# Kernel tuning notes

Measured on AMD Instinct MI355X. Metric: run time of the kernel, lower is better.

## Reference

```python
import jax, jax.numpy as jnp
import numpy as np

N_VIDEOS = 256
EMBED_DIM = 1024
MARGIN = 0.0

def _segment_sizes():
    i = np.arange(N_VIDEOS)
    num_clips = 8 + (i % 17)            # sum = 4088
    num_caps = 8 + ((5 * i + 3) % 17)   # sum = 4091
    return num_clips, num_caps

def setup_inputs() -> dict:
    key = jax.random.key(0)
    num_clips, num_caps = _segment_sizes()
    total_clips = int(num_clips.sum())
    total_caps = int(num_caps.sum())
    k1, k2 = jax.random.split(key)
    im = jax.random.normal(k1, (total_clips, EMBED_DIM), dtype=jnp.float32)
    s = jax.random.normal(k2, (total_caps, EMBED_DIM), dtype=jnp.float32)
    return {
        "im": im,
        "s": s,
        "num_clips": jnp.asarray(num_clips, jnp.int32),
        "num_caps": jnp.asarray(num_caps, jnp.int32),
    }

def reference(im, s, num_clips, num_caps):
    N = num_clips.shape[0]
    # full similarity matrix [total_clips, total_caps]
    scores = im @ s.T
    # segment ids mapping each clip/caption row to its video group
    clip_seg = jnp.repeat(jnp.arange(N), num_clips, total_repeat_length=im.shape[0])
    cap_seg = jnp.repeat(jnp.arange(N), num_caps, total_repeat_length=s.shape[0])
    # two-stage segmented sum -> block sums [N, N], then divide for block means
    row_red = jax.ops.segment_sum(scores, clip_seg, num_segments=N)       # [N, total_caps]
    blk_sum = jax.ops.segment_sum(row_red.T, cap_seg, num_segments=N).T   # [N, N]
    counts = num_clips.astype(jnp.float32)[:, None] * num_caps.astype(jnp.float32)[None, :]
    S = blk_sum / counts
    diag = jnp.diag(S)
    cost_s = jnp.maximum(MARGIN + S - diag[:, None], 0.0)   # caption retrieval
    cost_im = jnp.maximum(MARGIN + S - diag[None, :], 0.0)  # image retrieval
    eye = jnp.eye(N, dtype=bool)
    cost_s = jnp.where(eye, 0.0, cost_s)
    cost_im = jnp.where(eye, 0.0, cost_im)
    return cost_s.sum() + cost_im.sum()
```

## Files before the change

kernel.cpp:

```cpp
#include <hip/hip_runtime.h>

#define NVID 256
#define DIM 1024

__device__ inline void acc4(float4& a, const float4& v) {
    a.x += v.x; a.y += v.y; a.z += v.z; a.w += v.w;
}

__global__ __launch_bounds__(256) void seg_mean_kernel(
    const float* __restrict__ im, const float* __restrict__ s,
    const int* __restrict__ num_clips, const int* __restrict__ num_caps,
    float* __restrict__ A, float* __restrict__ B, float* __restrict__ out)
{
    const int b = blockIdx.x;
    const int t = threadIdx.x;
    if (b == 0 && t == 0) out[0] = 0.0f;

    const bool isClip = (b < NVID);
    const int vid = isClip ? b : b - NVID;
    const int* cnt = isClip ? num_clips : num_caps;
    const float* src = isClip ? im : s;
    float* dst = isClip ? A : B;

    __shared__ int scnt[NVID];
    scnt[t] = cnt[t];
    __syncthreads();

    int off = 0;
    for (int k = 0; k < vid; ++k) off += scnt[k];
    const int n = scnt[vid];

    const float4* srcv = (const float4*)src + (size_t)off * (DIM / 4) + t;
    float4 a0 = {0,0,0,0}, a1 = {0,0,0,0}, a2 = {0,0,0,0}, a3 = {0,0,0,0};
    int r = 0;
    for (; r + 4 <= n; r += 4) {
        float4 v0 = srcv[(size_t)(r + 0) * (DIM / 4)];
        float4 v1 = srcv[(size_t)(r + 1) * (DIM / 4)];
        float4 v2 = srcv[(size_t)(r + 2) * (DIM / 4)];
        float4 v3 = srcv[(size_t)(r + 3) * (DIM / 4)];
        acc4(a0, v0); acc4(a1, v1); acc4(a2, v2); acc4(a3, v3);
    }
    for (; r < n; ++r) {
        float4 v = srcv[(size_t)r * (DIM / 4)];
        acc4(a0, v);
    }
    acc4(a0, a1); acc4(a2, a3); acc4(a0, a2);
    const float inv = 1.0f / (float)n;
    a0.x *= inv; a0.y *= inv; a0.z *= inv; a0.w *= inv;
    ((float4*)(dst + (size_t)vid * DIM))[t] = a0;
}

__global__ __launch_bounds__(256) void diag_kernel(
    const float* __restrict__ A, const float* __restrict__ B,
    float* __restrict__ diag)
{
    const int i = blockIdx.x;
    const int t = threadIdx.x;
    float4 a = ((const float4*)(A + (size_t)i * DIM))[t];
    float4 b = ((const float4*)(B + (size_t)i * DIM))[t];
    float p = a.x * b.x + a.y * b.y + a.z * b.z + a.w * b.w;

    for (int o = 32; o > 0; o >>= 1) p += __shfl_down(p, o, 64);

    __shared__ float wsum[4];
    const int wave = t >> 6, lane = t & 63;
    if (lane == 0) wsum[wave] = p;
    __syncthreads();
    if (t == 0) diag[i] = wsum[0] + wsum[1] + wsum[2] + wsum[3];
}

__global__ __launch_bounds__(256) void loss_kernel(
    const float* __restrict__ A, const float* __restrict__ B,
    const float* __restrict__ diag, float* __restrict__ out)
{
    constexpr int KC = 64;
    constexpr int LDW = KC + 4;
    __shared__ float As[2][16][LDW];
    __shared__ float Bs[2][16][LDW];

    const int t = threadIdx.x;
    const int tx = t & 15, ty = t >> 4;
    const int i0 = blockIdx.y * 16, j0 = blockIdx.x * 16;

    const int lrow = t >> 4;
    const int lcol = (t & 15) * 4;

    const float* Arow = A + (size_t)(i0 + lrow) * DIM + lcol;
    const float* Brow = B + (size_t)(j0 + lrow) * DIM + lcol;

    float4 va = *(const float4*)(Arow + 0);
    float4 vb = *(const float4*)(Brow + 0);
    *(float4*)&As[0][lrow][lcol] = va;
    *(float4*)&Bs[0][lrow][lcol] = vb;
    __syncthreads();

    float acc = 0.f;
    constexpr int NCHUNK = DIM / KC;
    for (int c = 0; c < NCHUNK; ++c) {
        const int cur = c & 1;
        if (c + 1 < NCHUNK) {
            va = *(const float4*)(Arow + (c + 1) * KC);
            vb = *(const float4*)(Brow + (c + 1) * KC);
        }
#pragma unroll
        for (int k = 0; k < KC; k += 4) {
            float4 fa = *(const float4*)&As[cur][ty][k];
            float4 fb = *(const float4*)&Bs[cur][tx][k];
            acc += fa.x * fb.x + fa.y * fb.y + fa.z * fb.z + fa.w * fb.w;
        }
        if (c + 1 < NCHUNK) {
            *(float4*)&As[cur ^ 1][lrow][lcol] = va;
            *(float4*)&Bs[cur ^ 1][lrow][lcol] = vb;
        }
        __syncthreads();
    }

    const int i = i0 + ty, j = j0 + tx;
    float v = 0.f;
    if (i != j) {
        const float dI = diag[i];
        const float dJ = diag[j];
        v = fmaxf(acc - dI, 0.f) + fmaxf(acc - dJ, 0.f);
    }

    for (int o = 32; o > 0; o >>= 1) v += __shfl_down(v, o, 64);
    __shared__ float wsum[4];
    const int wave = t >> 6, lane = t & 63;
    if (lane == 0) wsum[wave] = v;
    __syncthreads();
    if (t == 0) atomicAdd(out, wsum[0] + wsum[1] + wsum[2] + wsum[3]);
}

extern "C" void kernel_launch(void* const* d_in, const int* in_sizes, int n_in,
                              void* d_out, int out_size, void* d_ws, size_t ws_size,
                              hipStream_t stream) {
    const float* im    = (const float*)d_in[0];
    const float* s     = (const float*)d_in[1];
    const int*   nclip = (const int*)d_in[2];
    const int*   ncap  = (const int*)d_in[3];
    float* out = (float*)d_out;

    float* A    = (float*)d_ws;
    float* B    = A + NVID * DIM;
    float* diag = B + NVID * DIM;

    seg_mean_kernel<<<2 * NVID, 256, 0, stream>>>(im, s, nclip, ncap, A, B, out);
    diag_kernel<<<NVID, 256, 0, stream>>>(A, B, diag);
    loss_kernel<<<dim3(16, 16), 256, 0, stream>>>(A, B, diag, out);
}
```

Measured before the change: 95.53 us.

## Store segment means as bf16 and compute block scores with MFMA

Segment-mean rows are now stored in bf16, and the 256x256 score GEMM is done by one wave per 16x16 tile using the 16x16x32 bf16 MFMA instruction instead of an LDS-tiled FP32 dot-product loop. The diag kernel reads the same bf16 values, so diagonal and off-diagonal scores stay consistent. The segment-mean loop is also unrolled to eight rows per iteration. The aim is less workspace traffic and faster matrix-core math in the loss kernel. The cost is bf16 rounding of the means, which may perturb the hinge sum since the margin is zero.

```diff
diff --git a/kernel.cpp b/kernel.cpp
--- a/kernel.cpp
+++ b/kernel.cpp
@@ -1,16 +1,32 @@
 #include <hip/hip_runtime.h>
+#include <hip/hip_bf16.h>
 
 #define NVID 256
 #define DIM 1024
+
+typedef short bf16x8 __attribute__((ext_vector_type(8)));
+typedef float f32x4 __attribute__((ext_vector_type(4)));
 
 __device__ inline void acc4(float4& a, const float4& v) {
     a.x += v.x; a.y += v.y; a.z += v.z; a.w += v.w;
 }
 
+__device__ inline unsigned short f2bf(float f) {
+    __hip_bfloat16 h = __float2bfloat16(f);
+    unsigned short u;
+    __builtin_memcpy(&u, &h, 2);
+    return u;
+}
+
+__device__ inline float bf2f(unsigned short u) {
+    return __uint_as_float(((unsigned)u) << 16);
+}
+
 __global__ __launch_bounds__(256) void seg_mean_kernel(
     const float* __restrict__ im, const float* __restrict__ s,
     const int* __restrict__ num_clips, const int* __restrict__ num_caps,
-    float* __restrict__ A, float* __restrict__ B, float* __restrict__ out)
+    unsigned short* __restrict__ Ab, unsigned short* __restrict__ Bb,
+    float* __restrict__ out)
 {
     const int b = blockIdx.x;
     const int t = threadIdx.x;
@@ -20,7 +36,7 @@
     const int vid = isClip ? b : b - NVID;
     const int* cnt = isClip ? num_clips : num_caps;
     const float* src = isClip ? im : s;
-    float* dst = isClip ? A : B;
+    unsigned short* dst = isClip ? Ab : Bb;
 
     __shared__ int scnt[NVID];
     scnt[t] = cnt[t];
@@ -33,12 +49,17 @@
     const float4* srcv = (const float4*)src + (size_t)off * (DIM / 4) + t;
     float4 a0 = {0,0,0,0}, a1 = {0,0,0,0}, a2 = {0,0,0,0}, a3 = {0,0,0,0};
     int r = 0;
-    for (; r + 4 <= n; r += 4) {
+    for (; r + 8 <= n; r += 8) {
         float4 v0 = srcv[(size_t)(r + 0) * (DIM / 4)];
         float4 v1 = srcv[(size_t)(r + 1) * (DIM / 4)];
         float4 v2 = srcv[(size_t)(r + 2) * (DIM / 4)];
         float4 v3 = srcv[(size_t)(r + 3) * (DIM / 4)];
+        float4 v4 = srcv[(size_t)(r + 4) * (DIM / 4)];
+        float4 v5 = srcv[(size_t)(r + 5) * (DIM / 4)];
+        float4 v6 = srcv[(size_t)(r + 6) * (DIM / 4)];
+        float4 v7 = srcv[(size_t)(r + 7) * (DIM / 4)];
         acc4(a0, v0); acc4(a1, v1); acc4(a2, v2); acc4(a3, v3);
+        acc4(a0, v4); acc4(a1, v5); acc4(a2, v6); acc4(a3, v7);
     }
     for (; r < n; ++r) {
         float4 v = srcv[(size_t)r * (DIM / 4)];
@@ -47,18 +68,22 @@
     acc4(a0, a1); acc4(a2, a3); acc4(a0, a2);
     const float inv = 1.0f / (float)n;
     a0.x *= inv; a0.y *= inv; a0.z *= inv; a0.w *= inv;
-    ((float4*)(dst + (size_t)vid * DIM))[t] = a0;
+
+    ushort4 ov;
+    ov.x = f2bf(a0.x); ov.y = f2bf(a0.y); ov.z = f2bf(a0.z); ov.w = f2bf(a0.w);
+    ((ushort4*)(dst + (size_t)vid * DIM))[t] = ov;
 }
 
 __global__ __launch_bounds__(256) void diag_kernel(
-    const float* __restrict__ A, const float* __restrict__ B,
+    const unsigned short* __restrict__ Ab, const unsigned short* __restrict__ Bb,
     float* __restrict__ diag)
 {
     const int i = blockIdx.x;
     const int t = threadIdx.x;
-    float4 a = ((const float4*)(A + (size_t)i * DIM))[t];
-    float4 b = ((const float4*)(B + (size_t)i * DIM))[t];
-    float p = a.x * b.x + a.y * b.y + a.z * b.z + a.w * b.w;
+    ushort4 ua = ((const ushort4*)(Ab + (size_t)i * DIM))[t];
+    ushort4 ub = ((const ushort4*)(Bb + (size_t)i * DIM))[t];
+    float p = bf2f(ua.x) * bf2f(ub.x) + bf2f(ua.y) * bf2f(ub.y)
+            + bf2f(ua.z) * bf2f(ub.z) + bf2f(ua.w) * bf2f(ub.w);
 
     for (int o = 32; o > 0; o >>= 1) p += __shfl_down(p, o, 64);
 
@@ -69,66 +94,42 @@
     if (t == 0) diag[i] = wsum[0] + wsum[1] + wsum[2] + wsum[3];
 }
 
-__global__ __launch_bounds__(256) void loss_kernel(
-    const float* __restrict__ A, const float* __restrict__ B,
+__global__ __launch_bounds__(64) void loss_kernel(
+    const unsigned short* __restrict__ Ab, const unsigned short* __restrict__ Bb,
     const float* __restrict__ diag, float* __restrict__ out)
 {
-    constexpr int KC = 64;
-    constexpr int LDW = KC + 4;
-    __shared__ float As[2][16][LDW];
-    __shared__ float Bs[2][16][LDW];
+    const int lane = threadIdx.x;
+    const int i0 = blockIdx.y * 16, j0 = blockIdx.x * 16;
+    const int m = lane & 15, q = lane >> 4;
 
-    const int t = threadIdx.x;
-    const int tx = t & 15, ty = t >> 4;
-    const int i0 = blockIdx.y * 16, j0 = blockIdx.x * 16;
+    const unsigned short* Ap = Ab + (size_t)(i0 + m) * DIM + q * 8;
+    const unsigned short* Bp = Bb + (size_t)(j0 + m) * DIM + q * 8;
 
-    const int lrow = t >> 4;
-    const int lcol = (t & 15) * 4;
-
-    const float* Arow = A + (size_t)(i0 + lrow) * DIM + lcol;
-    const float* Brow = B + (size_t)(j0 + lrow) * DIM + lcol;
-
-    float4 va = *(const float4*)(Arow + 0);
-    float4 vb = *(const float4*)(Brow + 0);
-    *(float4*)&As[0][lrow][lcol] = va;
-    *(float4*)&Bs[0][lrow][lcol] = vb;
-    __syncthreads();
-
-    float acc = 0.f;
-    constexpr int NCHUNK = DIM / KC;
-    for (int c = 0; c < NCHUNK; ++c) {
-        const int cur = c & 1;
-        if (c + 1 < NCHUNK) {
-            va = *(const float4*)(Arow + (c + 1) * KC);
-            vb = *(const float4*)(Brow + (c + 1) * KC);
-        }
+    f32x4 acc = {0.f, 0.f, 0.f, 0.f};
 #pragma unroll
-        for (int k = 0; k < KC; k += 4) {
-            float4 fa = *(const float4*)&As[cur][ty][k];
-            float4 fb = *(const float4*)&Bs[cur][tx][k];
-            acc += fa.x * fb.x + fa.y * fb.y + fa.z * fb.z + fa.w * fb.w;
-        }
-        if (c + 1 < NCHUNK) {
-            *(float4*)&As[cur ^ 1][lrow][lcol] = va;
-            *(float4*)&Bs[cur ^ 1][lrow][lcol] = vb;
-        }
-        __syncthreads();
+    for (int kb = 0; kb < DIM; kb += 32) {
+        bf16x8 a = *(const bf16x8*)(Ap + kb);
+        bf16x8 b = *(const bf16x8*)(Bp + kb);
+        acc = __builtin_amdgcn_mfma_f32_16x16x32_bf16(a, b, acc, 0, 0, 0);
     }
 
-    const int i = i0 + ty, j = j0 + tx;
+    const int j = j0 + m;
+    const float dj = diag[j];
+    const float4 di = *(const float4*)&diag[i0 + q * 4];
+    const float dia[4] = {di.x, di.y, di.z, di.w};
+
     float v = 0.f;
-    if (i != j) {
-        const float dI = diag[i];
-        const float dJ = diag[j];
-        v = fmaxf(acc - dI, 0.f) + fmaxf(acc - dJ, 0.f);
+#pragma unroll
+    for (int r = 0; r < 4; ++r) {
+        const int i = i0 + q * 4 + r;
+        if (i != j) {
+            const float sv = acc[r];
+            v += fmaxf(sv - dia[r], 0.f) + fmaxf(sv - dj, 0.f);
+        }
     }
 
     for (int o = 32; o > 0; o >>= 1) v += __shfl_down(v, o, 64);
-    __shared__ float wsum[4];
-    const int wave = t >> 6, lane = t & 63;
-    if (lane == 0) wsum[wave] = v;
-    __syncthreads();
-    if (t == 0) atomicAdd(out, wsum[0] + wsum[1] + wsum[2] + wsum[3]);
+    if (lane == 0) atomicAdd(out, v);
 }
 
 extern "C" void kernel_launch(void* const* d_in, const int* in_sizes, int n_in,
@@ -140,11 +141,11 @@
     const int*   ncap  = (const int*)d_in[3];
     float* out = (float*)d_out;
 
-    float* A    = (float*)d_ws;
-    float* B    = A + NVID * DIM;
-    float* diag = B + NVID * DIM;
+    unsigned short* Ab = (unsigned short*)d_ws;
+    unsigned short* Bb = Ab + NVID * DIM;
+    float* diag = (float*)(Bb + NVID * DIM);
 
-    seg_mean_kernel<<<2 * NVID, 256, 0, stream>>>(im, s, nclip, ncap, A, B, out);
-    diag_kernel<<<NVID, 256, 0, stream>>>(A, B, diag);
-    loss_kernel<<<dim3(16, 16), 256, 0, stream>>>(A, B, diag, out);
+    seg_mean_kernel<<<2 * NVID, 256, 0, stream>>>(im, s, nclip, ncap, Ab, Bb, out);
+    diag_kernel<<<NVID, 256, 0, stream>>>(Ab, Bb, diag);
+    loss_kernel<<<dim3(16, 16), 64, 0, stream>>>(Ab, Bb, diag, out);
 }
```

Result: faster. 87.47 us (-8.4%).
